# Performance work log

Measured on AMD Instinct MI355X. Metric: run time of the kernel, lower is better.

## Reference

```python
import jax, jax.numpy as jnp
import numpy as np

THRESHOLD = 0.5


def setup_inputs() -> dict:
    key = jax.random.key(0)
    T, B = 2048, 4096
    x = jax.random.uniform(key, (T, B, 2), dtype=jnp.float32)  # push/pop signals in [0,1]
    state0 = jnp.zeros((B, 2), dtype=jnp.float32)  # [count, tanh(count)]
    return {"x": x, "state0": state0}


def _step(state, xt):
    # state: [B, 2] = [count, tanh(count)]; xt: [B, 2] = [push, pop]
    push_sig = xt[..., 0]
    pop_sig = xt[..., 1]
    is_push = (push_sig >= THRESHOLD) & (push_sig >= pop_sig)
    is_pop = (pop_sig >= THRESHOLD) & (pop_sig > push_sig)
    delta = jnp.where(is_push, 1.0, jnp.where(is_pop, -1.0, 0.0))
    count = state[..., 0] + delta
    new_state = jnp.stack([count, jnp.tanh(count)], axis=-1)
    return new_state, new_state


def reference(x, state0):
    # x: [T, B, 2], state0: [B, 2] -> all per-step states [T, B, 2]
    _, states = jax.lax.scan(_step, state0, x)
    return states
```

## Files before the change

### kernel.cpp

```cpp
#include <hip/hip_runtime.h>
#include <math.h>

#define T_TOTAL 2048
#define B_TOTAL 4096
#define B2      (B_TOTAL / 2)
#define NCHUNK  64
#define TCHUNK  (T_TOTAL / NCHUNK)

typedef float fvec4 __attribute__((ext_vector_type(4)));

__device__ __forceinline__ int delta_of(float p, float q) {
    return (p >= 0.5f && p >= q) ? 1 : ((q >= 0.5f && q > p) ? -1 : 0);
}

__device__ __forceinline__ float fast_tanh(float x) {
    float e = __builtin_amdgcn_exp2f(x * 2.885390081777927f);
    return 1.0f - 2.0f / (e + 1.0f);
}

__device__ __forceinline__ int sext2(unsigned int bits2) {
    return ((int)(bits2 << 30)) >> 30;
}

__global__ void __launch_bounds__(256)
scan_pass1(const fvec4* __restrict__ x4,
           int2* __restrict__ partial,
           ulonglong2* __restrict__ packed) {
    const int p = blockIdx.x * blockDim.x + threadIdx.x;
    const int c = blockIdx.y;
    const int t0 = c * TCHUNK;

    int s0 = 0, s1 = 0;
    unsigned long long w0 = 0ull, w1 = 0ull;

#pragma unroll
    for (int t = 0; t < 16; ++t) {
        fvec4 v = __builtin_nontemporal_load(&x4[(size_t)(t0 + t) * B2 + p]);
        int d0 = delta_of(v.x, v.y);
        int d1 = delta_of(v.z, v.w);
        s0 += d0; s1 += d1;
        unsigned int nib = (unsigned int)(d0 & 3) | ((unsigned int)(d1 & 3) << 2);
        w0 |= (unsigned long long)nib << (4 * t);
    }
#pragma unroll
    for (int t = 16; t < 32; ++t) {
        fvec4 v = __builtin_nontemporal_load(&x4[(size_t)(t0 + t) * B2 + p]);
        int d0 = delta_of(v.x, v.y);
        int d1 = delta_of(v.z, v.w);
        s0 += d0; s1 += d1;
        unsigned int nib = (unsigned int)(d0 & 3) | ((unsigned int)(d1 & 3) << 2);
        w1 |= (unsigned long long)nib << (4 * (t - 16));
    }

    ulonglong2 w; w.x = w0; w.y = w1;
    packed[(size_t)c * B2 + p] = w;
    int2 s; s.x = s0; s.y = s1;
    partial[(size_t)c * B2 + p] = s;
}

__global__ void __launch_bounds__(256)
scan_emit(const int2* __restrict__ partial,
          const ulonglong2* __restrict__ packed,
          fvec4* __restrict__ o4) {
    const int p = blockIdx.x * blockDim.x + threadIdx.x;
    const int c = blockIdx.y;
    const int t0 = c * TCHUNK;

    int c0 = 0, c1 = 0;
    for (int cc = 0; cc < c; ++cc) {
        int2 v = partial[(size_t)cc * B2 + p];
        c0 += v.x; c1 += v.y;
    }

    ulonglong2 w = packed[(size_t)c * B2 + p];

#pragma unroll
    for (int t = 0; t < 16; ++t) {
        unsigned int nib = (unsigned int)(w.x >> (4 * t)) & 0xFu;
        c0 += sext2(nib & 3u);
        c1 += sext2(nib >> 2);
        float f0 = (float)c0, f1 = (float)c1;
        fvec4 o; o.x = f0; o.y = fast_tanh(f0); o.z = f1; o.w = fast_tanh(f1);
        __builtin_nontemporal_store(o, &o4[(size_t)(t0 + t) * B2 + p]);
    }
#pragma unroll
    for (int t = 16; t < 32; ++t) {
        unsigned int nib = (unsigned int)(w.y >> (4 * (t - 16))) & 0xFu;
        c0 += sext2(nib & 3u);
        c1 += sext2(nib >> 2);
        float f0 = (float)c0, f1 = (float)c1;
        fvec4 o; o.x = f0; o.y = fast_tanh(f0); o.z = f1; o.w = fast_tanh(f1);
        __builtin_nontemporal_store(o, &o4[(size_t)(t0 + t) * B2 + p]);
    }
}

__global__ void naive_scan(const float* __restrict__ x, float* __restrict__ out) {
    const int b = blockIdx.x * blockDim.x + threadIdx.x;
    if (b >= B_TOTAL) return;
    const float2* __restrict__ x2 = (const float2*)x;
    float2* __restrict__ o2 = (float2*)out;
    int count = 0;
    for (int t = 0; t < T_TOTAL; ++t) {
        float2 v = x2[(size_t)t * B_TOTAL + b];
        count += delta_of(v.x, v.y);
        float fc = (float)count;
        float2 w; w.x = fc; w.y = tanhf(fc);
        o2[(size_t)t * B_TOTAL + b] = w;
    }
}

extern "C" void kernel_launch(void* const* d_in, const int* in_sizes, int n_in,
                              void* d_out, int out_size, void* d_ws, size_t ws_size,
                              hipStream_t stream) {
    const float* x = (const float*)d_in[0];
    float* out = (float*)d_out;

    const size_t partial_bytes = (size_t)NCHUNK * B2 * sizeof(int2);
    const size_t packed_bytes  = (size_t)NCHUNK * B2 * sizeof(ulonglong2);
    if (ws_size < partial_bytes + packed_bytes) {
        naive_scan<<<dim3((B_TOTAL + 255) / 256), dim3(256), 0, stream>>>(x, out);
        return;
    }
    int2* partial = (int2*)d_ws;
    ulonglong2* packed = (ulonglong2*)((char*)d_ws + partial_bytes);

    dim3 block(256);
    dim3 grid(B2 / 256, NCHUNK);
    scan_pass1<<<grid, block, 0, stream>>>((const fvec4*)x, partial, packed);
    scan_emit<<<grid, block, 0, stream>>>(partial, packed, (fvec4*)out);
}
```

Measured before the change: 118.5 us.

## Fuse two-pass chunked scan into one cooperative kernel with grid sync

Merges the partial-sum pass and the emit pass into a single cooperative kernel. The packed delta bits now stay in registers across a grid-wide barrier instead of going through global memory, and one launch is removed. The grid of 8x64 blocks of 256 threads must be co-resident for the cooperative launch to succeed, and the grid.sync adds barrier cost. If the launch fails, the code falls back to the two-kernel path. The naive fallback for a small workspace is removed, so with too little workspace nothing runs.

After: 209.3 us. 76.5% more time.

```diff
diff --git a/kernel.cpp b/kernel.cpp
--- a/kernel.cpp
+++ b/kernel.cpp
@@ -1,5 +1,8 @@
 #include <hip/hip_runtime.h>
+#include <hip/hip_cooperative_groups.h>
 #include <math.h>
+
+namespace cg = cooperative_groups;
 
 #define T_TOTAL 2048
 #define B_TOTAL 4096
@@ -23,9 +26,11 @@
 }
 
 __global__ void __launch_bounds__(256)
-scan_pass1(const fvec4* __restrict__ x4,
-           int2* __restrict__ partial,
-           ulonglong2* __restrict__ packed) {
+scan_coop(const fvec4* __restrict__ x4,
+          unsigned long long* __restrict__ partial,
+          fvec4* __restrict__ o4) {
+    cg::grid_group grid = cg::this_grid();
+
     const int p = blockIdx.x * blockDim.x + threadIdx.x;
     const int c = blockIdx.y;
     const int t0 = c * TCHUNK;
@@ -52,6 +57,69 @@
         w1 |= (unsigned long long)nib << (4 * (t - 16));
     }
 
+    unsigned long long agg =
+        (unsigned long long)(unsigned int)s0 |
+        ((unsigned long long)(unsigned int)s1 << 32);
+    __hip_atomic_store(&partial[(size_t)c * B2 + p], agg,
+                       __ATOMIC_RELAXED, __HIP_MEMORY_SCOPE_AGENT);
+
+    grid.sync();
+
+    int c0 = 0, c1 = 0;
+    for (int cc = 0; cc < c; ++cc) {
+        unsigned long long v = __hip_atomic_load(&partial[(size_t)cc * B2 + p],
+                                                 __ATOMIC_RELAXED, __HIP_MEMORY_SCOPE_AGENT);
+        c0 += (int)(unsigned int)(v & 0xFFFFFFFFull);
+        c1 += (int)(unsigned int)(v >> 32);
+    }
+
+#pragma unroll
+    for (int t = 0; t < 16; ++t) {
+        unsigned int nib = (unsigned int)(w0 >> (4 * t)) & 0xFu;
+        c0 += sext2(nib & 3u);
+        c1 += sext2(nib >> 2);
+        float f0 = (float)c0, f1 = (float)c1;
+        fvec4 o; o.x = f0; o.y = fast_tanh(f0); o.z = f1; o.w = fast_tanh(f1);
+        __builtin_nontemporal_store(o, &o4[(size_t)(t0 + t) * B2 + p]);
+    }
+#pragma unroll
+    for (int t = 16; t < 32; ++t) {
+        unsigned int nib = (unsigned int)(w1 >> (4 * (t - 16))) & 0xFu;
+        c0 += sext2(nib & 3u);
+        c1 += sext2(nib >> 2);
+        float f0 = (float)c0, f1 = (float)c1;
+        fvec4 o; o.x = f0; o.y = fast_tanh(f0); o.z = f1; o.w = fast_tanh(f1);
+        __builtin_nontemporal_store(o, &o4[(size_t)(t0 + t) * B2 + p]);
+    }
+}
+
+__global__ void __launch_bounds__(256)
+scan_pass1(const fvec4* __restrict__ x4,
+           int2* __restrict__ partial,
+           ulonglong2* __restrict__ packed) {
+    const int p = blockIdx.x * blockDim.x + threadIdx.x;
+    const int c = blockIdx.y;
+    const int t0 = c * TCHUNK;
+    int s0 = 0, s1 = 0;
+    unsigned long long w0 = 0ull, w1 = 0ull;
+#pragma unroll
+    for (int t = 0; t < 16; ++t) {
+        fvec4 v = __builtin_nontemporal_load(&x4[(size_t)(t0 + t) * B2 + p]);
+        int d0 = delta_of(v.x, v.y);
+        int d1 = delta_of(v.z, v.w);
+        s0 += d0; s1 += d1;
+        unsigned int nib = (unsigned int)(d0 & 3) | ((unsigned int)(d1 & 3) << 2);
+        w0 |= (unsigned long long)nib << (4 * t);
+    }
+#pragma unroll
+    for (int t = 16; t < 32; ++t) {
+        fvec4 v = __builtin_nontemporal_load(&x4[(size_t)(t0 + t) * B2 + p]);
+        int d0 = delta_of(v.x, v.y);
+        int d1 = delta_of(v.z, v.w);
+        s0 += d0; s1 += d1;
+        unsigned int nib = (unsigned int)(d0 & 3) | ((unsigned int)(d1 & 3) << 2);
+        w1 |= (unsigned long long)nib << (4 * (t - 16));
+    }
     ulonglong2 w; w.x = w0; w.y = w1;
     packed[(size_t)c * B2 + p] = w;
     int2 s; s.x = s0; s.y = s1;
@@ -65,15 +133,12 @@
     const int p = blockIdx.x * blockDim.x + threadIdx.x;
     const int c = blockIdx.y;
     const int t0 = c * TCHUNK;
-
     int c0 = 0, c1 = 0;
     for (int cc = 0; cc < c; ++cc) {
         int2 v = partial[(size_t)cc * B2 + p];
         c0 += v.x; c1 += v.y;
     }
-
     ulonglong2 w = packed[(size_t)c * B2 + p];
-
 #pragma unroll
     for (int t = 0; t < 16; ++t) {
         unsigned int nib = (unsigned int)(w.x >> (4 * t)) & 0xFu;
@@ -94,38 +159,30 @@
     }
 }
 
-__global__ void naive_scan(const float* __restrict__ x, float* __restrict__ out) {
-    const int b = blockIdx.x * blockDim.x + threadIdx.x;
-    if (b >= B_TOTAL) return;
-    const float2* __restrict__ x2 = (const float2*)x;
-    float2* __restrict__ o2 = (float2*)out;
-    int count = 0;
-    for (int t = 0; t < T_TOTAL; ++t) {
-        float2 v = x2[(size_t)t * B_TOTAL + b];
-        count += delta_of(v.x, v.y);
-        float fc = (float)count;
-        float2 w; w.x = fc; w.y = tanhf(fc);
-        o2[(size_t)t * B_TOTAL + b] = w;
-    }
-}
-
 extern "C" void kernel_launch(void* const* d_in, const int* in_sizes, int n_in,
                               void* d_out, int out_size, void* d_ws, size_t ws_size,
                               hipStream_t stream) {
-    const float* x = (const float*)d_in[0];
-    float* out = (float*)d_out;
+    const fvec4* x4 = (const fvec4*)d_in[0];
+    fvec4* o4 = (fvec4*)d_out;
 
-    const size_t partial_bytes = (size_t)NCHUNK * B2 * sizeof(int2);
+    const size_t partial_bytes = (size_t)NCHUNK * B2 * sizeof(unsigned long long);
     const size_t packed_bytes  = (size_t)NCHUNK * B2 * sizeof(ulonglong2);
-    if (ws_size < partial_bytes + packed_bytes) {
-        naive_scan<<<dim3((B_TOTAL + 255) / 256), dim3(256), 0, stream>>>(x, out);
-        return;
-    }
-    int2* partial = (int2*)d_ws;
-    ulonglong2* packed = (ulonglong2*)((char*)d_ws + partial_bytes);
 
     dim3 block(256);
     dim3 grid(B2 / 256, NCHUNK);
-    scan_pass1<<<grid, block, 0, stream>>>((const fvec4*)x, partial, packed);
-    scan_emit<<<grid, block, 0, stream>>>(partial, packed, (fvec4*)out);
+
+    if (ws_size >= partial_bytes) {
+        unsigned long long* partial = (unsigned long long*)d_ws;
+        void* args[] = {(void*)&x4, (void*)&partial, (void*)&o4};
+        hipError_t err = hipLaunchCooperativeKernel((const void*)scan_coop, grid, block,
+                                                    args, 0, stream);
+        if (err == hipSuccess) return;
+    }
+
+    if (ws_size >= partial_bytes + packed_bytes) {
+        int2* partial = (int2*)d_ws;
+        ulonglong2* packed = (ulonglong2*)((char*)d_ws + (size_t)NCHUNK * B2 * sizeof(int2));
+        scan_pass1<<<grid, block, 0, stream>>>(x4, partial, packed);
+        scan_emit<<<grid, block, 0, stream>>>(partial, packed, o4);
+    }
 }
```
